# Kernel tuning notes

Hardware: AMD Instinct MI355X
Metric: run time of the kernel (lower is better)

The kernel has to match this reference:

```python
import jax, jax.numpy as jnp
import numpy as np

B, T, IN, H = 4096, 100, 140, 256


def setup_inputs() -> dict:
    key = jax.random.key(0)
    ks = jax.random.split(key, 13)
    s = 1.0 / np.sqrt(H)  # PyTorch LSTM/Linear default init scale
    u = lambda k, shape: jax.random.uniform(k, shape, jnp.float32, -s, s)
    return {
        "x": jax.random.normal(ks[0], (B, T, IN), jnp.float32),
        # LSTM layer 0 (input 140 -> hidden 256), PyTorch gate order i,f,g,o
        "W_ih0": u(ks[1], (4 * H, IN)),
        "W_hh0": u(ks[2], (4 * H, H)),
        "b_ih0": u(ks[3], (4 * H,)),
        "b_hh0": u(ks[4], (4 * H,)),
        # LSTM layer 1 (hidden 256 -> hidden 256)
        "W_ih1": u(ks[5], (4 * H, H)),
        "W_hh1": u(ks[6], (4 * H, H)),
        "b_ih1": u(ks[7], (4 * H,)),
        "b_hh1": u(ks[8], (4 * H,)),
        # advantage MLP: Linear(256,256) -> ReLU -> Linear(256,1)
        "W_a1": u(ks[9], (H, H)),
        "b_a1": u(ks[10], (H,)),
        "W_a2": u(ks[11], (1, H)),
        "b_a2": u(ks[12], (1,)),
    }


def _lstm_cell(xt, h, c, W_ih, W_hh, b):
    # xt: (B, in), h/c: (B, H). PyTorch gate order: i, f, g, o.
    g = xt @ W_ih.T + h @ W_hh.T + b
    i, f, gg, o = jnp.split(g, 4, axis=-1)
    c_new = jax.nn.sigmoid(f) * c + jax.nn.sigmoid(i) * jnp.tanh(gg)
    h_new = jax.nn.sigmoid(o) * jnp.tanh(c_new)
    return h_new, c_new


def reference(x, W_ih0, W_hh0, b_ih0, b_hh0, W_ih1, W_hh1, b_ih1, b_hh1,
              W_a1, b_a1, W_a2, b_a2):
    Bx = x.shape[0]
    b0 = b_ih0 + b_hh0
    b1 = b_ih1 + b_hh1

    def step(carry, xt):
        h0, c0, h1, c1 = carry
        h0, c0 = _lstm_cell(xt, h0, c0, W_ih0, W_hh0, b0)
        h1, c1 = _lstm_cell(h0, h1, c1, W_ih1, W_hh1, b1)
        a = jax.nn.relu(h1 @ W_a1.T + b_a1) @ W_a2.T + b_a2  # (B, 1)
        return (h0, c0, h1, c1), a[:, 0]

    init = tuple(jnp.zeros((Bx, H), x.dtype) for _ in range(4))
    _, outs = jax.lax.scan(step, init, jnp.swapaxes(x, 0, 1))  # (T, B)
    # Faithful to torch.cat(outputs).view(B, -1): flatten in t-major order,
    # then reshape to (B, T) (this scrambles batch/time exactly as the original).
    return outs.reshape(Bx, -1)
```

## Files before the change

kernel.cpp:

```cpp
#include <hip/hip_runtime.h>
#include <cstdint>
#include <cstddef>

#define T_STEPS 100
#define IN_DIM  140
#define HDIM    256
#define BTOT    4096
#define MROWS   16
#define NBLK    (BTOT/MROWS)
#define NTHR    512

typedef _Float16 f16;
typedef _Float16 f16x8 __attribute__((ext_vector_type(8)));
typedef float    f32x4 __attribute__((ext_vector_type(4)));

#define NS0 13
#define NS1 16
#define NSA 8
#define E0 (NS0*64*512)
#define E1 (NS1*64*512)
#define EA (NSA*16*512)
#define F16TOT (E0+E1+EA)
#define EB 2048
#define PREP_TOT (F16TOT+EB)

#define ACOLS 680
#define H0COL 160
#define H1COL 416

__device__ __forceinline__ float sigmoidf_(float x) {
    return 1.0f / (1.0f + __expf(-x));
}
__device__ __forceinline__ float tanhf_(float x) {
    return 1.0f - 2.0f / (__expf(2.0f * x) + 1.0f);
}

__global__ void prep(const float* __restrict__ Wih0, const float* __restrict__ Whh0,
                     const float* __restrict__ bih0, const float* __restrict__ bhh0,
                     const float* __restrict__ Wih1, const float* __restrict__ Whh1,
                     const float* __restrict__ bih1, const float* __restrict__ bhh1,
                     const float* __restrict__ Wa1,  f16* __restrict__ wsf,
                     float* __restrict__ wsb)
{
    int idx = blockIdx.x * 256 + threadIdx.x;
    if (idx < E0) {
        int e = idx & 7, l = (idx >> 3) & 63, fi = idx >> 9;
        int nt = fi & 63, ks = fi >> 6;
        int k = ks * 32 + ((l >> 4) << 3) + e;
        int n = nt * 16 + (l & 15);
        float v = (k < 160) ? (k < IN_DIM ? Wih0[n * IN_DIM + k] : 0.f)
                            : Whh0[n * HDIM + (k - 160)];
        wsf[idx] = (f16)v;
    } else if (idx < E0 + E1) {
        int i2 = idx - E0;
        int e = i2 & 7, l = (i2 >> 3) & 63, fi = i2 >> 9;
        int nt = fi & 63, ks = fi >> 6;
        int k = ks * 32 + ((l >> 4) << 3) + e;
        int n = nt * 16 + (l & 15);
        float v = (k < HDIM) ? Wih1[n * HDIM + k] : Whh1[n * HDIM + (k - HDIM)];
        wsf[idx] = (f16)v;
    } else if (idx < F16TOT) {
        int i3 = idx - (E0 + E1);
        int e = i3 & 7, l = (i3 >> 3) & 63, fi = i3 >> 9;
        int nt = fi & 15, ks = fi >> 4;
        int k = ks * 32 + ((l >> 4) << 3) + e;
        int j = nt * 16 + (l & 15);
        wsf[idx] = (f16)Wa1[j * HDIM + k];
    } else if (idx < PREP_TOT) {
        int i4 = idx - F16TOT;
        if (i4 < 1024) wsb[i4] = bih0[i4] + bhh0[i4];
        else           wsb[i4] = bih1[i4 - 1024] + bhh1[i4 - 1024];
    }
}

#define GLOAD_LDS(gsrc, ldst)                                              \
    __builtin_amdgcn_global_load_lds(                                      \
        (const __attribute__((address_space(1))) void*)(gsrc),             \
        (__attribute__((address_space(3))) void*)(ldst), 16, 0, 0)

__device__ __forceinline__ void stage8(const f16* slice, f16* dst, int w, int l) {
    #pragma unroll
    for (int g = 0; g < 4; g++)
        #pragma unroll
        for (int q = 0; q < 2; q++) {
            const f16* src = slice + (size_t)(g * 16 + 2 * w + q) * 512 + l * 8;
            GLOAD_LDS(src, dst + (g * 2 + q) * 512);
        }
}

__device__ __forceinline__ void stage2(const f16* slice, f16* dst, int w, int l) {
    #pragma unroll
    for (int q = 0; q < 2; q++) {
        const f16* src = slice + (size_t)(2 * w + q) * 512 + l * 8;
        GLOAD_LDS(src, dst + q * 512);
    }
}

#define WAIT_LGKM0 do { asm volatile("s_waitcnt lgkmcnt(0)" ::: "memory"); \
                        __builtin_amdgcn_sched_barrier(0); } while (0)
#define WAIT_VM(N) do { asm volatile("s_waitcnt vmcnt(" #N ")" ::: "memory"); \
                        __builtin_amdgcn_sched_barrier(0); } while (0)

__global__ __launch_bounds__(NTHR) void lstm_mfma(
    const float* __restrict__ x, const f16* __restrict__ wsf,
    const float* __restrict__ wsb, const float* __restrict__ Wa2,
    const float* __restrict__ ba1, const float* __restrict__ ba2,
    float* __restrict__ out)
{
    __shared__ __align__(16) f16 A[MROWS][ACOLS];
    __shared__ __align__(16) f16 Bst[8][2][4096];
    __shared__ float red[8][MROWS];

    const int tid = threadIdx.x;
    const int l   = tid & 63;
    const int w   = tid >> 6;
    const int lm  = l & 15;
    const int lk  = (l >> 4) << 3;
    const int m0  = (l >> 4) << 2;
    const int row0 = blockIdx.x * MROWS;

    const f16* W0 = wsf;
    const f16* W1 = wsf + E0;
    const f16* WA = wsf + E0 + E1;
    f16* wb0 = &Bst[w][0][0];
    f16* wb1 = &Bst[w][1][0];

    for (int i = tid; i < MROWS * ACOLS; i += NTHR) ((f16*)A)[i] = (f16)0.f;

    const int u0 = (2 * w) * 16 + lm;
    const int u1 = (2 * w + 1) * 16 + lm;
    float b0v[2][4], b1v[2][4];
    #pragma unroll
    for (int g = 0; g < 4; g++) {
        b0v[0][g] = wsb[g * 256 + u0];          b0v[1][g] = wsb[g * 256 + u1];
        b1v[0][g] = wsb[1024 + g * 256 + u0];   b1v[1][g] = wsb[1024 + g * 256 + u1];
    }
    const float bAv[2]  = { ba1[u0], ba1[u1] };
    const float wa2v[2] = { Wa2[u0], Wa2[u1] };
    const float ba2v    = ba2[0];

    float c0s[2][4], c1s[2][4];
    #pragma unroll
    for (int q = 0; q < 2; q++)
        #pragma unroll
        for (int r = 0; r < 4; r++) { c0s[q][r] = 0.f; c1s[q][r] = 0.f; }

    __syncthreads();

    #pragma unroll 1
    for (int t = 0; t < T_STEPS; t++) {
        for (int i = tid; i < MROWS * IN_DIM; i += NTHR) {
            int b = i / IN_DIM, k = i - b * IN_DIM;
            A[b][k] = (f16)x[(size_t)(row0 + b) * (T_STEPS * IN_DIM) + (size_t)t * IN_DIM + k];
        }
        __syncthreads();

        f32x4 acc[2][4];
        #pragma unroll
        for (int q = 0; q < 2; q++)
            #pragma unroll
            for (int g = 0; g < 4; g++) {
                float b = b0v[q][g];
                acc[q][g] = (f32x4){b, b, b, b};
            }
        stage8(W0, wb0, w, l);
        #pragma unroll 1
        for (int ks = 0; ks < NS0; ks++) {
            WAIT_LGKM0;
            if (ks + 1 < NS0) {
                stage8(W0 + (size_t)(ks + 1) * 64 * 512, (ks & 1) ? wb0 : wb1, w, l);
                WAIT_VM(8);
            } else {
                WAIT_VM(0);
            }
            const f16* rb = (ks & 1) ? wb1 : wb0;
            f16x8 a0 = *(const f16x8*)&A[lm][ks * 32 + lk];
            #pragma unroll
            for (int g = 0; g < 4; g++)
                #pragma unroll
                for (int q = 0; q < 2; q++) {
                    f16x8 bf = *(const f16x8*)(rb + (g * 2 + q) * 512 + l * 8);
                    acc[q][g] = __builtin_amdgcn_mfma_f32_16x16x32_f16(a0, bf, acc[q][g], 0, 0, 0);
                }
        }
        stage8(W1, wb0, w, l);

        f16 hnew[2][4];
        #pragma unroll
        for (int q = 0; q < 2; q++)
            #pragma unroll
            for (int r = 0; r < 4; r++) {
                float ig = sigmoidf_(acc[q][0][r]);
                float fg = sigmoidf_(acc[q][1][r]);
                float gv = tanhf_   (acc[q][2][r]);
                float og = sigmoidf_(acc[q][3][r]);
                float c  = fmaf(fg, c0s[q][r], ig * gv);
                c0s[q][r] = c;
                hnew[q][r] = (f16)(og * tanhf_(c));
            }
        __syncthreads();
        #pragma unroll
        for (int r = 0; r < 4; r++) {
            A[m0 + r][H0COL + u0] = hnew[0][r];
            A[m0 + r][H0COL + u1] = hnew[1][r];
        }
        __syncthreads();

        #pragma unroll
        for (int q = 0; q < 2; q++)
            #pragma unroll
            for (int g = 0; g < 4; g++) {
                float b = b1v[q][g];
                acc[q][g] = (f32x4){b, b, b, b};
            }
        #pragma unroll 1
        for (int ks = 0; ks < NS1; ks++) {
            WAIT_LGKM0;
            if (ks + 1 < NS1) {
                stage8(W1 + (size_t)(ks + 1) * 64 * 512, (ks & 1) ? wb0 : wb1, w, l);
                WAIT_VM(8);
            } else {
                WAIT_VM(0);
            }
            const f16* rb = (ks & 1) ? wb1 : wb0;
            f16x8 a0 = *(const f16x8*)&A[lm][H0COL + ks * 32 + lk];
            #pragma unroll
            for (int g = 0; g < 4; g++)
                #pragma unroll
                for (int q = 0; q < 2; q++) {
                    f16x8 bf = *(const f16x8*)(rb + (g * 2 + q) * 512 + l * 8);
                    acc[q][g] = __builtin_amdgcn_mfma_f32_16x16x32_f16(a0, bf, acc[q][g], 0, 0, 0);
                }
        }
        stage2(WA, wb0, w, l);

        #pragma unroll
        for (int q = 0; q < 2; q++)
            #pragma unroll
            for (int r = 0; r < 4; r++) {
                float ig = sigmoidf_(acc[q][0][r]);
                float fg = sigmoidf_(acc[q][1][r]);
                float gv = tanhf_   (acc[q][2][r]);
                float og = sigmoidf_(acc[q][3][r]);
                float c  = fmaf(fg, c1s[q][r], ig * gv);
                c1s[q][r] = c;
                hnew[q][r] = (f16)(og * tanhf_(c));
            }
        __syncthreads();
        #pragma unroll
        for (int r = 0; r < 4; r++) {
            A[m0 + r][H1COL + u0] = hnew[0][r];
            A[m0 + r][H1COL + u1] = hnew[1][r];
        }
        __syncthreads();

        f32x4 accA[2];
        #pragma unroll
        for (int q = 0; q < 2; q++) {
            float b = bAv[q];
            accA[q] = (f32x4){b, b, b, b};
        }
        #pragma unroll 1
        for (int ks = 0; ks < NSA; ks++) {
            WAIT_LGKM0;
            if (ks + 1 < NSA) {
                stage2(WA + (size_t)(ks + 1) * 16 * 512, (ks & 1) ? wb0 : wb1, w, l);
                WAIT_VM(2);
            } else {
                WAIT_VM(0);
            }
            const f16* rb = (ks & 1) ? wb1 : wb0;
            f16x8 a0 = *(const f16x8*)&A[lm][H1COL + ks * 32 + lk];
            #pragma unroll
            for (int q = 0; q < 2; q++) {
                f16x8 bf = *(const f16x8*)(rb + q * 512 + l * 8);
                accA[q] = __builtin_amdgcn_mfma_f32_16x16x32_f16(a0, bf, accA[q], 0, 0, 0);
            }
        }
        float s[4];
        #pragma unroll
        for (int r = 0; r < 4; r++)
            s[r] = fmaxf(accA[0][r], 0.f) * wa2v[0] + fmaxf(accA[1][r], 0.f) * wa2v[1];
        #pragma unroll
        for (int msk = 1; msk < 16; msk <<= 1)
            #pragma unroll
            for (int r = 0; r < 4; r++)
                s[r] += __shfl_xor(s[r], msk, 64);
        if (lm == 0) {
            #pragma unroll
            for (int r = 0; r < 4; r++) red[w][m0 + r] = s[r];
        }
        __syncthreads();
        if (tid < MROWS) {
            float o = ba2v;
            #pragma unroll
            for (int w2 = 0; w2 < 8; w2++) o += red[w2][tid];
            out[(size_t)t * BTOT + row0 + tid] = o;
        }
    }
}

extern "C" void kernel_launch(void* const* d_in, const int* in_sizes, int n_in,
                              void* d_out, int out_size, void* d_ws, size_t ws_size,
                              hipStream_t stream)
{
    const float* x    = (const float*)d_in[0];
    const float* Wih0 = (const float*)d_in[1];
    const float* Whh0 = (const float*)d_in[2];
    const float* bih0 = (const float*)d_in[3];
    const float* bhh0 = (const float*)d_in[4];
    const float* Wih1 = (const float*)d_in[5];
    const float* Whh1 = (const float*)d_in[6];
    const float* bih1 = (const float*)d_in[7];
    const float* bhh1 = (const float*)d_in[8];
    const float* Wa1  = (const float*)d_in[9];
    const float* ba1  = (const float*)d_in[10];
    const float* Wa2  = (const float*)d_in[11];
    const float* ba2  = (const float*)d_in[12];

    f16*   wsf = (f16*)d_ws;
    float* wsb = (float*)((char*)d_ws + (size_t)F16TOT * sizeof(f16));
    float* out = (float*)d_out;

    hipLaunchKernelGGL(prep, dim3(PREP_TOT / 256), dim3(256), 0, stream,
                       Wih0, Whh0, bih0, bhh0, Wih1, Whh1, bih1, bhh1, Wa1, wsf, wsb);
    hipLaunchKernelGGL(lstm_mfma, dim3(NBLK), dim3(NTHR), 0, stream,
                       x, wsf, wsb, Wa2, ba1, ba2, out);
}
```

Before: 2.205 ms.

## Double batch rows per block and split hidden units across sixteen waves

Each block now handles 32 batch rows with 1024 threads, and each of the 16 waves owns one 16-unit hidden slice across two M-tiles. Every staged weight fragment therefore feeds two MFMAs, halving weight traffic per row and the number of blocks. Weight staging moves to a three-slot ring of half-steps (two gates each) with a prefetch distance of two. The cost is fewer blocks (128) on a large GPU, which may leave CUs idle, plus heavier barriers among 16 waves.

Result: slower. 2.894 ms (+31.3%).

```diff
diff --git a/kernel.cpp b/kernel.cpp
--- a/kernel.cpp
+++ b/kernel.cpp
@@ -6,9 +6,9 @@
 #define IN_DIM  140
 #define HDIM    256
 #define BTOT    4096
-#define MROWS   16
+#define MROWS   32
 #define NBLK    (BTOT/MROWS)
-#define NTHR    512
+#define NTHR    1024
 
 typedef _Float16 f16;
 typedef _Float16 f16x8 __attribute__((ext_vector_type(8)));
@@ -17,6 +17,8 @@
 #define NS0 13
 #define NS1 16
 #define NSA 8
+#define NH0 (2*NS0)
+#define NH1 (2*NS1)
 #define E0 (NS0*64*512)
 #define E1 (NS1*64*512)
 #define EA (NSA*16*512)
@@ -78,27 +80,12 @@
         (const __attribute__((address_space(1))) void*)(gsrc),             \
         (__attribute__((address_space(3))) void*)(ldst), 16, 0, 0)
 
-__device__ __forceinline__ void stage8(const f16* slice, f16* dst, int w, int l) {
-    #pragma unroll
-    for (int g = 0; g < 4; g++)
-        #pragma unroll
-        for (int q = 0; q < 2; q++) {
-            const f16* src = slice + (size_t)(g * 16 + 2 * w + q) * 512 + l * 8;
-            GLOAD_LDS(src, dst + (g * 2 + q) * 512);
-        }
-}
-
-__device__ __forceinline__ void stage2(const f16* slice, f16* dst, int w, int l) {
-    #pragma unroll
-    for (int q = 0; q < 2; q++) {
-        const f16* src = slice + (size_t)(2 * w + q) * 512 + l * 8;
-        GLOAD_LDS(src, dst + q * 512);
-    }
-}
-
+template<int N>
+__device__ __forceinline__ void wait_vm() {
+    asm volatile("s_waitcnt vmcnt(%0)" :: "i"(N) : "memory");
+    __builtin_amdgcn_sched_barrier(0);
+}
 #define WAIT_LGKM0 do { asm volatile("s_waitcnt lgkmcnt(0)" ::: "memory"); \
-                        __builtin_amdgcn_sched_barrier(0); } while (0)
-#define WAIT_VM(N) do { asm volatile("s_waitcnt vmcnt(" #N ")" ::: "memory"); \
                         __builtin_amdgcn_sched_barrier(0); } while (0)
 
 __global__ __launch_bounds__(NTHR) void lstm_mfma(
@@ -108,8 +95,8 @@
     float* __restrict__ out)
 {
     __shared__ __align__(16) f16 A[MROWS][ACOLS];
-    __shared__ __align__(16) f16 Bst[8][2][4096];
-    __shared__ float red[8][MROWS];
+    __shared__ __align__(16) f16 Bst[16][3][1024];
+    __shared__ float red[16][MROWS];
 
     const int tid = threadIdx.x;
     const int l   = tid & 63;
@@ -122,28 +109,26 @@
     const f16* W0 = wsf;
     const f16* W1 = wsf + E0;
     const f16* WA = wsf + E0 + E1;
-    f16* wb0 = &Bst[w][0][0];
-    f16* wb1 = &Bst[w][1][0];
+    f16* wbuf = &Bst[w][0][0];
 
     for (int i = tid; i < MROWS * ACOLS; i += NTHR) ((f16*)A)[i] = (f16)0.f;
 
-    const int u0 = (2 * w) * 16 + lm;
-    const int u1 = (2 * w + 1) * 16 + lm;
-    float b0v[2][4], b1v[2][4];
+    const int u = w * 16 + lm;
+    float b0v[4], b1v[4];
     #pragma unroll
     for (int g = 0; g < 4; g++) {
-        b0v[0][g] = wsb[g * 256 + u0];          b0v[1][g] = wsb[g * 256 + u1];
-        b1v[0][g] = wsb[1024 + g * 256 + u0];   b1v[1][g] = wsb[1024 + g * 256 + u1];
+        b0v[g] = wsb[g * 256 + u];
+        b1v[g] = wsb[1024 + g * 256 + u];
     }
-    const float bAv[2]  = { ba1[u0], ba1[u1] };
-    const float wa2v[2] = { Wa2[u0], Wa2[u1] };
-    const float ba2v    = ba2[0];
+    const float bAv  = ba1[u];
+    const float wa2v = Wa2[u];
+    const float ba2v = ba2[0];
 
     float c0s[2][4], c1s[2][4];
     #pragma unroll
-    for (int q = 0; q < 2; q++)
-        #pragma unroll
-        for (int r = 0; r < 4; r++) { c0s[q][r] = 0.f; c1s[q][r] = 0.f; }
+    for (int mt = 0; mt < 2; mt++)
+        #pragma unroll
+        for (int r = 0; r < 4; r++) { c0s[mt][r] = 0.f; c1s[mt][r] = 0.f; }
 
     __syncthreads();
 
@@ -157,144 +142,229 @@
 
         f32x4 acc[2][4];
         #pragma unroll
-        for (int q = 0; q < 2; q++)
+        for (int mt = 0; mt < 2; mt++)
             #pragma unroll
             for (int g = 0; g < 4; g++) {
-                float b = b0v[q][g];
-                acc[q][g] = (f32x4){b, b, b, b};
-            }
-        stage8(W0, wb0, w, l);
+                float b = b0v[g];
+                acc[mt][g] = (f32x4){b, b, b, b};
+            }
+        WAIT_LGKM0;
+        #pragma unroll
+        for (int d = 0; d < 2; d++)
+            GLOAD_LDS(W0 + ((size_t)(0 * 64 + d * 16 + w)) * 512 + l * 8, wbuf + d * 512);
+        #pragma unroll
+        for (int d = 0; d < 2; d++)
+            GLOAD_LDS(W0 + ((size_t)(0 * 64 + (2 + d) * 16 + w)) * 512 + l * 8, wbuf + 1024 + d * 512);
+
+        f16x8 a0, a1;
         #pragma unroll 1
         for (int ks = 0; ks < NS0; ks++) {
-            WAIT_LGKM0;
-            if (ks + 1 < NS0) {
-                stage8(W0 + (size_t)(ks + 1) * 64 * 512, (ks & 1) ? wb0 : wb1, w, l);
-                WAIT_VM(8);
-            } else {
-                WAIT_VM(0);
-            }
-            const f16* rb = (ks & 1) ? wb1 : wb0;
-            f16x8 a0 = *(const f16x8*)&A[lm][ks * 32 + lk];
-            #pragma unroll
-            for (int g = 0; g < 4; g++)
-                #pragma unroll
-                for (int q = 0; q < 2; q++) {
-                    f16x8 bf = *(const f16x8*)(rb + (g * 2 + q) * 512 + l * 8);
-                    acc[q][g] = __builtin_amdgcn_mfma_f32_16x16x32_f16(a0, bf, acc[q][g], 0, 0, 0);
+            {
+                const int h = 2 * ks;
+                WAIT_LGKM0;
+                if (h + 2 < NH0) {
+                    const int hs = h + 2, kss = hs >> 1, gb = (hs & 1) * 2;
+                    f16* db = wbuf + ((hs % 3) << 10);
+                    #pragma unroll
+                    for (int d = 0; d < 2; d++)
+                        GLOAD_LDS(W0 + ((size_t)(kss * 64 + (gb + d) * 16 + w)) * 512 + l * 8, db + d * 512);
+                    wait_vm<4>();
+                } else {
+                    wait_vm<2>();
                 }
-        }
-        stage8(W1, wb0, w, l);
+                a0 = *(const f16x8*)&A[lm     ][ks * 32 + lk];
+                a1 = *(const f16x8*)&A[16 + lm][ks * 32 + lk];
+                const f16* rb = wbuf + ((h % 3) << 10);
+                f16x8 bf0 = *(const f16x8*)(rb + l * 8);
+                f16x8 bf1 = *(const f16x8*)(rb + 512 + l * 8);
+                acc[0][0] = __builtin_amdgcn_mfma_f32_16x16x32_f16(a0, bf0, acc[0][0], 0, 0, 0);
+                acc[1][0] = __builtin_amdgcn_mfma_f32_16x16x32_f16(a1, bf0, acc[1][0], 0, 0, 0);
+                acc[0][1] = __builtin_amdgcn_mfma_f32_16x16x32_f16(a0, bf1, acc[0][1], 0, 0, 0);
+                acc[1][1] = __builtin_amdgcn_mfma_f32_16x16x32_f16(a1, bf1, acc[1][1], 0, 0, 0);
+            }
+            {
+                const int h = 2 * ks + 1;
+                WAIT_LGKM0;
+                if (h + 2 < NH0) {
+                    const int hs = h + 2, kss = hs >> 1, gb = (hs & 1) * 2;
+                    f16* db = wbuf + ((hs % 3) << 10);
+                    #pragma unroll
+                    for (int d = 0; d < 2; d++)
+                        GLOAD_LDS(W0 + ((size_t)(kss * 64 + (gb + d) * 16 + w)) * 512 + l * 8, db + d * 512);
+                    wait_vm<4>();
+                } else if (h + 1 < NH0) {
+                    wait_vm<2>();
+                } else {
+                    wait_vm<0>();
+                }
+                const f16* rb = wbuf + ((h % 3) << 10);
+                f16x8 bf0 = *(const f16x8*)(rb + l * 8);
+                f16x8 bf1 = *(const f16x8*)(rb + 512 + l * 8);
+                acc[0][2] = __builtin_amdgcn_mfma_f32_16x16x32_f16(a0, bf0, acc[0][2], 0, 0, 0);
+                acc[1][2] = __builtin_amdgcn_mfma_f32_16x16x32_f16(a1, bf0, acc[1][2], 0, 0, 0);
+                acc[0][3] = __builtin_amdgcn_mfma_f32_16x16x32_f16(a0, bf1, acc[0][3], 0, 0, 0);
+                acc[1][3] = __builtin_amdgcn_mfma_f32_16x16x32_f16(a1, bf1, acc[1][3], 0, 0, 0);
+            }
+        }
+        WAIT_LGKM0;
+        #pragma unroll
+        for (int d = 0; d < 2; d++)
+            GLOAD_LDS(W1 + ((size_t)(d * 16 + w)) * 512 + l * 8, wbuf + d * 512);
+        #pragma unroll
+        for (int d = 0; d < 2; d++)
+            GLOAD_LDS(W1 + ((size_t)((2 + d) * 16 + w)) * 512 + l * 8, wbuf + 1024 + d * 512);
 
         f16 hnew[2][4];
         #pragma unroll
-        for (int q = 0; q < 2; q++)
+        for (int mt = 0; mt < 2; mt++)
             #pragma unroll
             for (int r = 0; r < 4; r++) {
-                float ig = sigmoidf_(acc[q][0][r]);
-                float fg = sigmoidf_(acc[q][1][r]);
-                float gv = tanhf_   (acc[q][2][r]);
-                float og = sigmoidf_(acc[q][3][r]);
-                float c  = fmaf(fg, c0s[q][r], ig * gv);
-                c0s[q][r] = c;
-                hnew[q][r] = (f16)(og * tanhf_(c));
-            }
-        __syncthreads();
-        #pragma unroll
-        for (int r = 0; r < 4; r++) {
-            A[m0 + r][H0COL + u0] = hnew[0][r];
-            A[m0 + r][H0COL + u1] = hnew[1][r];
-        }
-        __syncthreads();
-
-        #pragma unroll
-        for (int q = 0; q < 2; q++)
+                float ig = sigmoidf_(acc[mt][0][r]);
+                float fg = sigmoidf_(acc[mt][1][r]);
+                float gv = tanhf_   (acc[mt][2][r]);
+                float og = sigmoidf_(acc[mt][3][r]);
+                float c  = fmaf(fg, c0s[mt][r], ig * gv);
+                c0s[mt][r] = c;
+                hnew[mt][r] = (f16)(og * tanhf_(c));
+            }
+        __syncthreads();
+        #pragma unroll
+        for (int mt = 0; mt < 2; mt++)
+            #pragma unroll
+            for (int r = 0; r < 4; r++)
+                A[mt * 16 + m0 + r][H0COL + u] = hnew[mt][r];
+        __syncthreads();
+
+        #pragma unroll
+        for (int mt = 0; mt < 2; mt++)
             #pragma unroll
             for (int g = 0; g < 4; g++) {
-                float b = b1v[q][g];
-                acc[q][g] = (f32x4){b, b, b, b};
+                float b = b1v[g];
+                acc[mt][g] = (f32x4){b, b, b, b};
             }
         #pragma unroll 1
         for (int ks = 0; ks < NS1; ks++) {
-            WAIT_LGKM0;
-            if (ks + 1 < NS1) {
-                stage8(W1 + (size_t)(ks + 1) * 64 * 512, (ks & 1) ? wb0 : wb1, w, l);
-                WAIT_VM(8);
-            } else {
-                WAIT_VM(0);
-            }
-            const f16* rb = (ks & 1) ? wb1 : wb0;
-            f16x8 a0 = *(const f16x8*)&A[lm][H0COL + ks * 32 + lk];
-            #pragma unroll
-            for (int g = 0; g < 4; g++)
-                #pragma unroll
-                for (int q = 0; q < 2; q++) {
-                    f16x8 bf = *(const f16x8*)(rb + (g * 2 + q) * 512 + l * 8);
-                    acc[q][g] = __builtin_amdgcn_mfma_f32_16x16x32_f16(a0, bf, acc[q][g], 0, 0, 0);
+            {
+                const int h = 2 * ks;
+                WAIT_LGKM0;
+                if (h + 2 < NH1) {
+                    const int hs = h + 2, kss = hs >> 1, gb = (hs & 1) * 2;
+                    f16* db = wbuf + ((hs % 3) << 10);
+                    #pragma unroll
+                    for (int d = 0; d < 2; d++)
+                        GLOAD_LDS(W1 + ((size_t)(kss * 64 + (gb + d) * 16 + w)) * 512 + l * 8, db + d * 512);
+                    wait_vm<4>();
+                } else {
+                    wait_vm<2>();
                 }
-        }
-        stage2(WA, wb0, w, l);
-
-        #pragma unroll
-        for (int q = 0; q < 2; q++)
+                a0 = *(const f16x8*)&A[lm     ][H0COL + ks * 32 + lk];
+                a1 = *(const f16x8*)&A[16 + lm][H0COL + ks * 32 + lk];
+                const f16* rb = wbuf + ((h % 3) << 10);
+                f16x8 bf0 = *(const f16x8*)(rb + l * 8);
+                f16x8 bf1 = *(const f16x8*)(rb + 512 + l * 8);
+                acc[0][0] = __builtin_amdgcn_mfma_f32_16x16x32_f16(a0, bf0, acc[0][0], 0, 0, 0);
+                acc[1][0] = __builtin_amdgcn_mfma_f32_16x16x32_f16(a1, bf0, acc[1][0], 0, 0, 0);
+                acc[0][1] = __builtin_amdgcn_mfma_f32_16x16x32_f16(a0, bf1, acc[0][1], 0, 0, 0);
+                acc[1][1] = __builtin_amdgcn_mfma_f32_16x16x32_f16(a1, bf1, acc[1][1], 0, 0, 0);
+            }
+            {
+                const int h = 2 * ks + 1;
+                WAIT_LGKM0;
+                if (h + 2 < NH1) {
+                    const int hs = h + 2, kss = hs >> 1, gb = (hs & 1) * 2;
+                    f16* db = wbuf + ((hs % 3) << 10);
+                    #pragma unroll
+                    for (int d = 0; d < 2; d++)
+                        GLOAD_LDS(W1 + ((size_t)(kss * 64 + (gb + d) * 16 + w)) * 512 + l * 8, db + d * 512);
+                    wait_vm<4>();
+                } else if (h + 1 < NH1) {
+                    wait_vm<2>();
+                } else {
+                    wait_vm<0>();
+                }
+                const f16* rb = wbuf + ((h % 3) << 10);
+                f16x8 bf0 = *(const f16x8*)(rb + l * 8);
+                f16x8 bf1 = *(const f16x8*)(rb + 512 + l * 8);
+                acc[0][2] = __builtin_amdgcn_mfma_f32_16x16x32_f16(a0, bf0, acc[0][2], 0, 0, 0);
+                acc[1][2] = __builtin_amdgcn_mfma_f32_16x16x32_f16(a1, bf0, acc[1][2], 0, 0, 0);
+                acc[0][3] = __builtin_amdgcn_mfma_f32_16x16x32_f16(a0, bf1, acc[0][3], 0, 0, 0);
+                acc[1][3] = __builtin_amdgcn_mfma_f32_16x16x32_f16(a1, bf1, acc[1][3], 0, 0, 0);
+            }
+        }
+        WAIT_LGKM0;
+        GLOAD_LDS(WA + ((size_t)(0 * 16 + w)) * 512 + l * 8, wbuf);
+        GLOAD_LDS(WA + ((size_t)(1 * 16 + w)) * 512 + l * 8, wbuf + 1024);
+
+        #pragma unroll
+        for (int mt = 0; mt < 2; mt++)
             #pragma unroll
             for (int r = 0; r < 4; r++) {
-                float ig = sigmoidf_(acc[q][0][r]);
-                float fg = sigmoidf_(acc[q][1][r]);
-                float gv = tanhf_   (acc[q][2][r]);
-                float og = sigmoidf_(acc[q][3][r]);
-                float c  = fmaf(fg, c1s[q][r], ig * gv);
-                c1s[q][r] = c;
-                hnew[q][r] = (f16)(og * tanhf_(c));
-            }
-        __syncthreads();
-        #pragma unroll
-        for (int r = 0; r < 4; r++) {
-            A[m0 + r][H1COL + u0] = hnew[0][r];
-            A[m0 + r][H1COL + u1] = hnew[1][r];
-        }
+                float ig = sigmoidf_(acc[mt][0][r]);
+                float fg = sigmoidf_(acc[mt][1][r]);
+                float gv = tanhf_   (acc[mt][2][r]);
+                float og = sigmoidf_(acc[mt][3][r]);
+                float c  = fmaf(fg, c1s[mt][r], ig * gv);
+                c1s[mt][r] = c;
+                hnew[mt][r] = (f16)(og * tanhf_(c));
+            }
+        __syncthreads();
+        #pragma unroll
+        for (int mt = 0; mt < 2; mt++)
+            #pragma unroll
+            for (int r = 0; r < 4; r++)
+                A[mt * 16 + m0 + r][H1COL + u] = hnew[mt][r];
         __syncthreads();
 
         f32x4 accA[2];
         #pragma unroll
-        for (int q = 0; q < 2; q++) {
-            float b = bAv[q];
-            accA[q] = (f32x4){b, b, b, b};
+        for (int mt = 0; mt < 2; mt++) {
+            float b = bAv;
+            accA[mt] = (f32x4){b, b, b, b};
         }
         #pragma unroll 1
         for (int ks = 0; ks < NSA; ks++) {
             WAIT_LGKM0;
-            if (ks + 1 < NSA) {
-                stage2(WA + (size_t)(ks + 1) * 16 * 512, (ks & 1) ? wb0 : wb1, w, l);
-                WAIT_VM(2);
+            if (ks + 2 < NSA) {
+                GLOAD_LDS(WA + ((size_t)((ks + 2) * 16 + w)) * 512 + l * 8,
+                          wbuf + (((ks + 2) % 3) << 10));
+                wait_vm<2>();
+            } else if (ks + 1 < NSA) {
+                wait_vm<1>();
             } else {
-                WAIT_VM(0);
-            }
-            const f16* rb = (ks & 1) ? wb1 : wb0;
-            f16x8 a0 = *(const f16x8*)&A[lm][H1COL + ks * 32 + lk];
-            #pragma unroll
-            for (int q = 0; q < 2; q++) {
-                f16x8 bf = *(const f16x8*)(rb + q * 512 + l * 8);
-                accA[q] = __builtin_amdgcn_mfma_f32_16x16x32_f16(a0, bf, accA[q], 0, 0, 0);
-            }
-        }
-        float s[4];
-        #pragma unroll
-        for (int r = 0; r < 4; r++)
-            s[r] = fmaxf(accA[0][r], 0.f) * wa2v[0] + fmaxf(accA[1][r], 0.f) * wa2v[1];
+                wait_vm<0>();
+            }
+            f16x8 aa0 = *(const f16x8*)&A[lm     ][H1COL + ks * 32 + lk];
+            f16x8 aa1 = *(const f16x8*)&A[16 + lm][H1COL + ks * 32 + lk];
+            const f16* rb = wbuf + ((ks % 3) << 10);
+            f16x8 bf = *(const f16x8*)(rb + l * 8);
+            accA[0] = __builtin_amdgcn_mfma_f32_16x16x32_f16(aa0, bf, accA[0], 0, 0, 0);
+            accA[1] = __builtin_amdgcn_mfma_f32_16x16x32_f16(aa1, bf, accA[1], 0, 0, 0);
+        }
+        float s[2][4];
+        #pragma unroll
+        for (int mt = 0; mt < 2; mt++)
+            #pragma unroll
+            for (int r = 0; r < 4; r++)
+                s[mt][r] = fmaxf(accA[mt][r], 0.f) * wa2v;
         #pragma unroll
         for (int msk = 1; msk < 16; msk <<= 1)
             #pragma unroll
-            for (int r = 0; r < 4; r++)
-                s[r] += __shfl_xor(s[r], msk, 64);
+            for (int mt = 0; mt < 2; mt++)
+                #pragma unroll
+                for (int r = 0; r < 4; r++)
+                    s[mt][r] += __shfl_xor(s[mt][r], msk, 64);
         if (lm == 0) {
             #pragma unroll
-            for (int r = 0; r < 4; r++) red[w][m0 + r] = s[r];
+            for (int mt = 0; mt < 2; mt++)
+                #pragma unroll
+                for (int r = 0; r < 4; r++)
+                    red[w][mt * 16 + m0 + r] = s[mt][r];
         }
         __syncthreads();
         if (tid < MROWS) {
             float o = ba2v;
             #pragma unroll
-            for (int w2 = 0; w2 < 8; w2++) o += red[w2][tid];
+            for (int w2 = 0; w2 < 16; w2++) o += red[w2][tid];
             out[(size_t)t * BTOT + row0 + tid] = o;
         }
     }
```

## Pipeline weight staging across layers and steps, keep advantage weights in registers

Applied to the files above, without the earlier changes.

Weight streaming now runs continuously across phases. The last k-slice of layer 0 prefetches layer 1's first slice, and the last slice of layer 1 prefetches the next timestep's layer 0, with buffer parity chosen per step. The advantage-MLP weights are loaded once into registers, so their LDS staging disappears. The next timestep's x load is hoisted into the current step before the reduction, and __syncthreads is replaced by a raw s_barrier with an lgkm wait. This adds register pressure (16 f16x8 vectors) and relies on careful vmcnt and barrier ordering for correctness.

Result: no change. 2.162 ms (-1.9%).

```diff
diff --git a/kernel.cpp b/kernel.cpp
--- a/kernel.cpp
+++ b/kernel.cpp
@@ -88,18 +88,17 @@
         }
 }
 
-__device__ __forceinline__ void stage2(const f16* slice, f16* dst, int w, int l) {
-    #pragma unroll
-    for (int q = 0; q < 2; q++) {
-        const f16* src = slice + (size_t)(2 * w + q) * 512 + l * 8;
-        GLOAD_LDS(src, dst + q * 512);
-    }
-}
-
+template<int N>
+__device__ __forceinline__ void wait_vm() {
+    asm volatile("s_waitcnt vmcnt(%0)" :: "i"(N) : "memory");
+    __builtin_amdgcn_sched_barrier(0);
+}
 #define WAIT_LGKM0 do { asm volatile("s_waitcnt lgkmcnt(0)" ::: "memory"); \
                         __builtin_amdgcn_sched_barrier(0); } while (0)
-#define WAIT_VM(N) do { asm volatile("s_waitcnt vmcnt(" #N ")" ::: "memory"); \
-                        __builtin_amdgcn_sched_barrier(0); } while (0)
+#define BAR_LG do { asm volatile("s_waitcnt lgkmcnt(0)" ::: "memory");     \
+                    __builtin_amdgcn_sched_barrier(0);                     \
+                    __builtin_amdgcn_s_barrier();                          \
+                    __builtin_amdgcn_sched_barrier(0); } while (0)
 
 __global__ __launch_bounds__(NTHR) void lstm_mfma(
     const float* __restrict__ x, const f16* __restrict__ wsf,
@@ -122,8 +121,7 @@
     const f16* W0 = wsf;
     const f16* W1 = wsf + E0;
     const f16* WA = wsf + E0 + E1;
-    f16* wb0 = &Bst[w][0][0];
-    f16* wb1 = &Bst[w][1][0];
+    f16* wbuf = &Bst[w][0][0];
 
     for (int i = tid; i < MROWS * ACOLS; i += NTHR) ((f16*)A)[i] = (f16)0.f;
 
@@ -139,6 +137,13 @@
     const float wa2v[2] = { Wa2[u0], Wa2[u1] };
     const float ba2v    = ba2[0];
 
+    f16x8 advw[16];
+    #pragma unroll
+    for (int ks = 0; ks < NSA; ks++) {
+        advw[2 * ks + 0] = *(const f16x8*)(WA + (size_t)(ks * 16 + 2 * w + 0) * 512 + l * 8);
+        advw[2 * ks + 1] = *(const f16x8*)(WA + (size_t)(ks * 16 + 2 * w + 1) * 512 + l * 8);
+    }
+
     float c0s[2][4], c1s[2][4];
     #pragma unroll
     for (int q = 0; q < 2; q++)
@@ -147,13 +152,16 @@
 
     __syncthreads();
 
+    for (int i = tid; i < MROWS * IN_DIM; i += NTHR) {
+        int b = i / IN_DIM, k = i - b * IN_DIM;
+        A[b][k] = (f16)x[(size_t)(row0 + b) * (T_STEPS * IN_DIM) + k];
+    }
+    stage8(W0, wbuf, w, l);
+    __syncthreads();
+
     #pragma unroll 1
     for (int t = 0; t < T_STEPS; t++) {
-        for (int i = tid; i < MROWS * IN_DIM; i += NTHR) {
-            int b = i / IN_DIM, k = i - b * IN_DIM;
-            A[b][k] = (f16)x[(size_t)(row0 + b) * (T_STEPS * IN_DIM) + (size_t)t * IN_DIM + k];
-        }
-        __syncthreads();
+        const int p = t & 1;
 
         f32x4 acc[2][4];
         #pragma unroll
@@ -163,17 +171,16 @@
                 float b = b0v[q][g];
                 acc[q][g] = (f32x4){b, b, b, b};
             }
-        stage8(W0, wb0, w, l);
         #pragma unroll 1
         for (int ks = 0; ks < NS0; ks++) {
             WAIT_LGKM0;
-            if (ks + 1 < NS0) {
-                stage8(W0 + (size_t)(ks + 1) * 64 * 512, (ks & 1) ? wb0 : wb1, w, l);
-                WAIT_VM(8);
-            } else {
-                WAIT_VM(0);
-            }
-            const f16* rb = (ks & 1) ? wb1 : wb0;
+            {
+                f16* db = wbuf + (((ks + 1 + p) & 1) << 12);
+                if (ks < NS0 - 1) stage8(W0 + (size_t)(ks + 1) * 64 * 512, db, w, l);
+                else              stage8(W1, db, w, l);
+            }
+            wait_vm<8>();
+            const f16* rb = wbuf + (((ks + p) & 1) << 12);
             f16x8 a0 = *(const f16x8*)&A[lm][ks * 32 + lk];
             #pragma unroll
             for (int g = 0; g < 4; g++)
@@ -183,7 +190,6 @@
                     acc[q][g] = __builtin_amdgcn_mfma_f32_16x16x32_f16(a0, bf, acc[q][g], 0, 0, 0);
                 }
         }
-        stage8(W1, wb0, w, l);
 
         f16 hnew[2][4];
         #pragma unroll
@@ -198,13 +204,13 @@
                 c0s[q][r] = c;
                 hnew[q][r] = (f16)(og * tanhf_(c));
             }
-        __syncthreads();
+        BAR_LG;
         #pragma unroll
         for (int r = 0; r < 4; r++) {
             A[m0 + r][H0COL + u0] = hnew[0][r];
             A[m0 + r][H0COL + u1] = hnew[1][r];
         }
-        __syncthreads();
+        BAR_LG;
 
         #pragma unroll
         for (int q = 0; q < 2; q++)
@@ -216,13 +222,13 @@
         #pragma unroll 1
         for (int ks = 0; ks < NS1; ks++) {
             WAIT_LGKM0;
-            if (ks + 1 < NS1) {
-                stage8(W1 + (size_t)(ks + 1) * 64 * 512, (ks & 1) ? wb0 : wb1, w, l);
-                WAIT_VM(8);
-            } else {
-                WAIT_VM(0);
-            }
-            const f16* rb = (ks & 1) ? wb1 : wb0;
+            {
+                f16* db = wbuf + (((ks + p) & 1) << 12);
+                if (ks < NS1 - 1) stage8(W1 + (size_t)(ks + 1) * 64 * 512, db, w, l);
+                else              stage8(W0, db, w, l);
+            }
+            wait_vm<8>();
+            const f16* rb = wbuf + (((ks + 1 + p) & 1) << 12);
             f16x8 a0 = *(const f16x8*)&A[lm][H0COL + ks * 32 + lk];
             #pragma unroll
             for (int g = 0; g < 4; g++)
@@ -232,7 +238,6 @@
                     acc[q][g] = __builtin_amdgcn_mfma_f32_16x16x32_f16(a0, bf, acc[q][g], 0, 0, 0);
                 }
         }
-        stage2(WA, wb0, w, l);
 
         #pragma unroll
         for (int q = 0; q < 2; q++)
@@ -246,13 +251,13 @@
                 c1s[q][r] = c;
                 hnew[q][r] = (f16)(og * tanhf_(c));
             }
-        __syncthreads();
+        BAR_LG;
         #pragma unroll
         for (int r = 0; r < 4; r++) {
             A[m0 + r][H1COL + u0] = hnew[0][r];
             A[m0 + r][H1COL + u1] = hnew[1][r];
         }
-        __syncthreads();
+        BAR_LG;
 
         f32x4 accA[2];
         #pragma unroll
@@ -260,23 +265,21 @@
             float b = bAv[q];
             accA[q] = (f32x4){b, b, b, b};
         }
-        #pragma unroll 1
+        #pragma unroll
         for (int ks = 0; ks < NSA; ks++) {
-            WAIT_LGKM0;
-            if (ks + 1 < NSA) {
-                stage2(WA + (size_t)(ks + 1) * 16 * 512, (ks & 1) ? wb0 : wb1, w, l);
-                WAIT_VM(2);
-            } else {
-                WAIT_VM(0);
-            }
-            const f16* rb = (ks & 1) ? wb1 : wb0;
             f16x8 a0 = *(const f16x8*)&A[lm][H1COL + ks * 32 + lk];
-            #pragma unroll
-            for (int q = 0; q < 2; q++) {
-                f16x8 bf = *(const f16x8*)(rb + q * 512 + l * 8);
-                accA[q] = __builtin_amdgcn_mfma_f32_16x16x32_f16(a0, bf, accA[q], 0, 0, 0);
-            }
-        }
+            accA[0] = __builtin_amdgcn_mfma_f32_16x16x32_f16(a0, advw[2 * ks + 0], accA[0], 0, 0, 0);
+            accA[1] = __builtin_amdgcn_mfma_f32_16x16x32_f16(a0, advw[2 * ks + 1], accA[1], 0, 0, 0);
+        }
+
+        {
+            const int tn = (t + 1 < T_STEPS) ? (t + 1) : t;
+            for (int i = tid; i < MROWS * IN_DIM; i += NTHR) {
+                int b = i / IN_DIM, k = i - b * IN_DIM;
+                A[b][k] = (f16)x[(size_t)(row0 + b) * (T_STEPS * IN_DIM) + (size_t)tn * IN_DIM + k];
+            }
+        }
+
         float s[4];
         #pragma unroll
         for (int r = 0; r < 4; r++)
@@ -290,7 +293,7 @@
             #pragma unroll
             for (int r = 0; r < 4; r++) red[w][m0 + r] = s[r];
         }
-        __syncthreads();
+        BAR_LG;
         if (tid < MROWS) {
             float o = ba2v;
             #pragma unroll
```
